# Kernel tuning notes

Measured on AMD Instinct MI355X. Metric: run time of the kernel, lower is better.

The kernel has to match this reference:

```python
import jax, jax.numpy as jnp
import numpy as np

BATCH = 2
SEQ = 2048
D_MODEL = 512
D_STATE = 16
D_CONV = 4
D_INNER = 2 * D_MODEL  # expand=2


def setup_inputs() -> dict:
    key = jax.random.key(0)
    ks = jax.random.split(key, 7)
    s = 0.02
    x = jax.random.normal(ks[0], (BATCH, SEQ, D_MODEL), jnp.float32)
    W_in = jax.random.normal(ks[1], (2 * D_INNER, D_MODEL), jnp.float32) * s
    conv_w = jax.random.normal(ks[2], (D_INNER, 1, D_CONV), jnp.float32) * s  # depthwise kernel
    conv_b = jnp.zeros((D_INNER,), jnp.float32)
    W_x = jax.random.normal(ks[3], (2 * D_STATE, D_INNER), jnp.float32) * s
    W_dt = jax.random.normal(ks[4], (D_INNER, D_INNER), jnp.float32) * s
    b_dt = jnp.zeros((D_INNER,), jnp.float32)
    # A_log init: log of [1..d_state] broadcast over d_inner rows
    A_log = jnp.log(jnp.broadcast_to(jnp.arange(1, D_STATE + 1, dtype=jnp.float32), (D_INNER, D_STATE)))
    D_param = jnp.ones((D_INNER,), jnp.float32)
    W_out = jax.random.normal(ks[5], (D_MODEL, D_INNER), jnp.float32) * s
    return dict(x=x, W_in=W_in, conv_w=conv_w, conv_b=conv_b, W_x=W_x,
                W_dt=W_dt, b_dt=b_dt, A_log=A_log, D_param=D_param, W_out=W_out)


def reference(x, W_in, conv_w, conv_b, W_x, W_dt, b_dt, A_log, D_param, W_out):
    # in_proj, split into x-branch and gate z
    xz = x @ W_in.T                             # [B, L, 2*di]
    xi, z = jnp.split(xz, 2, axis=-1)
    # depthwise causal conv1d (torch pads both sides then slices [:seq_len] == left-pad only)
    h = jnp.transpose(xi, (0, 2, 1))            # [B, di, L]
    h = jax.lax.conv_general_dilated(
        h, conv_w, window_strides=(1,), padding=[(D_CONV - 1, 0)],
        dimension_numbers=('NCH', 'OIH', 'NCH'), feature_group_count=D_INNER)
    h = h + conv_b[None, :, None]
    h = jax.nn.silu(jnp.transpose(h, (0, 2, 1)))  # [B, L, di]

    A = -jnp.exp(A_log)                         # [di, ds]
    x_dbl = h @ W_x.T                           # [B, L, 2*ds]
    _delta_unused, Bmat = jnp.split(x_dbl, 2, axis=-1)  # B (also used as C): [B, L, ds]
    delta = jax.nn.softplus(h @ W_dt.T + b_dt)  # [B, L, di] (overwrites x_proj delta, as in source)

    def step(state, inp):
        d_t, B_t, h_t = inp                     # [B,di], [B,ds], [B,di]
        dA = jnp.exp(d_t[:, :, None] * A)       # [B, di, ds]
        state = dA * state + d_t[:, :, None] * B_t[:, None, :] * h_t[:, :, None]
        y_t = jnp.einsum('bds,bs->bd', state, B_t)  # C == B
        return state, y_t

    init = jnp.zeros((x.shape[0], D_INNER, D_STATE), x.dtype)
    _, ys = jax.lax.scan(step, init,
                         (jnp.swapaxes(delta, 0, 1), jnp.swapaxes(Bmat, 0, 1), jnp.swapaxes(h, 0, 1)))
    y = jnp.swapaxes(ys, 0, 1)                  # [B, L, di]
    y = (y + D_param * h) * jax.nn.silu(z)
    return y @ W_out.T                          # [B, L, d_model]
```

## Files before the change

### kernel.cpp

```cpp
#include <hip/hip_runtime.h>
#include <cstddef>
#include <cstdint>

#define NB 2
#define L_SEQ 2048
#define DM 512
#define DS 16
#define DI 1024
#define NC 64
#define CL (L_SEQ/NC)

typedef __attribute__((ext_vector_type(4))) float f32x4;
typedef __attribute__((ext_vector_type(8))) short bf16x8;

__device__ __forceinline__ float softplus_f(float x) {
  return (x > 20.f) ? x : log1pf(expf(x));
}
__device__ __forceinline__ float silu_f(float x) {
  return x / (1.f + expf(-x));
}
__device__ __forceinline__ ushort f2bf(float f) {
  uint32_t u = __float_as_uint(f);
  return (ushort)((u + 0x7fffu + ((u >> 16) & 1u)) >> 16);
}
__device__ __forceinline__ float bf2f(ushort h) {
  return __uint_as_float(((uint32_t)h) << 16);
}

__device__ __forceinline__ void gload16(const void* g, ushort* lds_wave_base) {
  __builtin_amdgcn_global_load_lds(
      (const __attribute__((address_space(1))) void*)g,
      (__attribute__((address_space(3))) void*)lds_wave_base, 16, 0, 0);
}

template <int N>
__device__ __forceinline__ void wait_vm() {
  if constexpr (N == 0)      asm volatile("s_waitcnt vmcnt(0)" ::: "memory");
  else if constexpr (N == 3) asm volatile("s_waitcnt vmcnt(3)" ::: "memory");
  else if constexpr (N == 4) asm volatile("s_waitcnt vmcnt(4)" ::: "memory");
  else if constexpr (N == 6) asm volatile("s_waitcnt vmcnt(6)" ::: "memory");
}

__global__ __launch_bounds__(256) void split_bf16(
    const float* __restrict__ in, ushort* __restrict__ hi,
    ushort* __restrict__ lo, int n4) {
  int i = blockIdx.x * 256 + threadIdx.x;
  if (i >= n4) return;
  float4 v = ((const float4*)in)[i];
  ushort h0 = f2bf(v.x), h1 = f2bf(v.y), h2 = f2bf(v.z), h3 = f2bf(v.w);
  ((ushort4*)hi)[i] = make_ushort4(h0, h1, h2, h3);
  ((ushort4*)lo)[i] = make_ushort4(
      f2bf(v.x - bf2f(h0)), f2bf(v.y - bf2f(h1)),
      f2bf(v.z - bf2f(h2)), f2bf(v.w - bf2f(h3)));
}

template <int ACT>
__global__ __launch_bounds__(512, 4) void gemm_mfma8(
    const ushort* __restrict__ Ahi, const ushort* __restrict__ Alo, int lda,
    const ushort* __restrict__ Bhi, const ushort* __restrict__ Blo, int ldb,
    const float* __restrict__ bias, float* __restrict__ C, int ldc, int K) {
  constexpr int BM = 128, BN = 64;
  constexpr int AT = BM * 32;
  constexpr int BT = BN * 32;
  constexpr int BUF = 2 * AT + 2 * BT;
  constexpr int MR = 2, NR = 2;
  __shared__ __align__(16) ushort lds[3 * BUF];

  const int tid = threadIdx.x;
  const int lane = tid & 63;
  const int wave = tid >> 6;
  const int wr = wave >> 1;
  const int wc = wave & 1;

  const int nx = gridDim.x;
  const int nwg = nx * gridDim.y;
  int bid = blockIdx.y * nx + blockIdx.x;
  bid = (bid & 7) * (nwg >> 3) + (bid >> 3);
  const int m0 = (bid / nx) * BM;
  const int n0 = (bid % nx) * BN;

  const int ra = tid >> 2;
  const int kga = (tid & 3) ^ ((ra >> 1) & 3);
  const size_t aoff = (size_t)(m0 + ra) * lda + kga * 8;
  const int tq = tid & 255;
  const int rb = tq >> 2;
  const int kgb = (tq & 3) ^ ((rb >> 1) & 3);
  const size_t boff = (size_t)(n0 + rb) * ldb + kgb * 8;
  const ushort* Bsel = (wave < 4) ? Bhi : Blo;
  const int blds = 2 * AT + ((wave < 4) ? wave * 512 : BT + (wave - 4) * 512);

  const int fr = lane & 15, fq = lane >> 4;
  const int kswz = fq ^ ((fr >> 1) & 3);
  int aoffs[MR], boffs[NR];
#pragma unroll
  for (int m = 0; m < MR; m++) aoffs[m] = (wr * 32 + m * 16 + fr) * 32 + kswz * 8;
#pragma unroll
  for (int n = 0; n < NR; n++) boffs[n] = (wc * 32 + n * 16 + fr) * 32 + kswz * 8;

  f32x4 acc[MR][NR];
#pragma unroll
  for (int m = 0; m < MR; m++)
#pragma unroll
    for (int n = 0; n < NR; n++) acc[m][n] = (f32x4){0.f, 0.f, 0.f, 0.f};

  const int nsteps = K >> 5;

#define STAGE(base, kk)                                     \
  {                                                         \
    ushort* bp = (base);                                    \
    gload16(Ahi + aoff + (kk), bp + wave * 512);            \
    gload16(Alo + aoff + (kk), bp + AT + wave * 512);       \
    gload16(Bsel + boff + (kk), bp + blds);                 \
  }

#define COMPUTE(base)                                                          \
  {                                                                            \
    const ushort* cp = (base);                                                 \
    bf16x8 ah[MR], al[MR], bh[NR], bl[NR];                                     \
    _Pragma("unroll")                                                          \
    for (int m = 0; m < MR; m++) ah[m] = *(const bf16x8*)(cp + aoffs[m]);      \
    _Pragma("unroll")                                                          \
    for (int m = 0; m < MR; m++) al[m] = *(const bf16x8*)(cp + AT + aoffs[m]); \
    _Pragma("unroll")                                                          \
    for (int n = 0; n < NR; n++) bh[n] = *(const bf16x8*)(cp + 2 * AT + boffs[n]); \
    _Pragma("unroll")                                                          \
    for (int n = 0; n < NR; n++) bl[n] = *(const bf16x8*)(cp + 2 * AT + BT + boffs[n]); \
    _Pragma("unroll")                                                          \
    for (int m = 0; m < MR; m++)                                               \
      _Pragma("unroll")                                                        \
      for (int n = 0; n < NR; n++)                                             \
        acc[m][n] = __builtin_amdgcn_mfma_f32_16x16x32_bf16(ah[m], bh[n], acc[m][n], 0, 0, 0); \
    _Pragma("unroll")                                                          \
    for (int m = 0; m < MR; m++)                                               \
      _Pragma("unroll")                                                        \
      for (int n = 0; n < NR; n++)                                             \
        acc[m][n] = __builtin_amdgcn_mfma_f32_16x16x32_bf16(al[m], bh[n], acc[m][n], 0, 0, 0); \
    _Pragma("unroll")                                                          \
    for (int m = 0; m < MR; m++)                                               \
      _Pragma("unroll")                                                        \
      for (int n = 0; n < NR; n++)                                             \
        acc[m][n] = __builtin_amdgcn_mfma_f32_16x16x32_bf16(ah[m], bl[n], acc[m][n], 0, 0, 0); \
  }

  STAGE(lds, 0);
  STAGE(lds + BUF, 32);
  int ocur = 0, onext = BUF, ofar = 2 * BUF;
  for (int t = 0; t < nsteps; ++t) {
    if (t == nsteps - 1) wait_vm<0>(); else wait_vm<3>();
    __builtin_amdgcn_s_barrier();
    if (t + 2 < nsteps) STAGE(lds + ofar, (t + 2) << 5);
    COMPUTE(lds + ocur);
    int tmp = ocur; ocur = onext; onext = ofar; ofar = tmp;
  }
#undef STAGE
#undef COMPUTE

#pragma unroll
  for (int m = 0; m < MR; m++) {
    const int row = m0 + wr * 32 + m * 16 + fq * 4;
#pragma unroll
    for (int n = 0; n < NR; n++) {
      const int col = n0 + wc * 32 + n * 16 + fr;
      float bcol = (ACT == 1) ? bias[col] : 0.f;
#pragma unroll
      for (int j = 0; j < 4; j++) {
        float v = acc[m][n][j];
        if (ACT == 1) v = softplus_f(v + bcol);
        C[(size_t)(row + j) * ldc + col] = v;
      }
    }
  }
}

template <int BM, int BN, int ACT>
__global__ __launch_bounds__(256) void gemm_mfma4(
    const ushort* __restrict__ Ahi, const ushort* __restrict__ Alo, int lda,
    const ushort* __restrict__ Bhi, const ushort* __restrict__ Blo, int ldb,
    const float* __restrict__ bias, float* __restrict__ C, int ldc, int K) {
  constexpr int AT = BM * 32;
  constexpr int BT = BN * 32;
  constexpr int BUF = 2 * AT + 2 * BT;
  constexpr int MR = BM / 32, NR = BN / 32;
  constexpr int LPS = (BM / 64) * 2 + (BN / 64) * 2;
  __shared__ __align__(16) ushort lds[3 * BUF];

  const int tid = threadIdx.x;
  const int lane = tid & 63;
  const int wave = tid >> 6;
  const int wr = wave >> 1, wc = wave & 1;

  const int nx = gridDim.x;
  const int nwg = nx * gridDim.y;
  int bid = blockIdx.y * nx + blockIdx.x;
  bid = (bid & 7) * (nwg >> 3) + (bid >> 3);
  const int m0 = (bid / nx) * BM;
  const int n0 = (bid % nx) * BN;

  const int r0 = tid >> 2;
  const int kg = (tid & 3) ^ ((r0 >> 1) & 3);
  const size_t aoff0 = (size_t)(m0 + r0) * lda + kg * 8;
  const size_t boff0 = (size_t)(n0 + r0) * ldb + kg * 8;

  const int fr = lane & 15, fq = lane >> 4;
  const int kswz = fq ^ ((fr >> 1) & 3);
  int aoffs[MR], boffs[NR];
#pragma unroll
  for (int m = 0; m < MR; m++) aoffs[m] = (wr * (BM / 2) + m * 16 + fr) * 32 + kswz * 8;
#pragma unroll
  for (int n = 0; n < NR; n++) boffs[n] = (wc * (BN / 2) + n * 16 + fr) * 32 + kswz * 8;

  f32x4 acc[MR][NR];
#pragma unroll
  for (int m = 0; m < MR; m++)
#pragma unroll
    for (int n = 0; n < NR; n++) acc[m][n] = (f32x4){0.f, 0.f, 0.f, 0.f};

  const int nsteps = K >> 5;

#define STAGE(base, kk)                                           \
  {                                                               \
    ushort* bp = (base);                                          \
    gload16(Ahi + aoff0 + (kk), bp + wave * 512);                 \
    gload16(Alo + aoff0 + (kk), bp + AT + wave * 512);            \
    gload16(Bhi + boff0 + (kk), bp + 2 * AT + wave * 512);        \
    gload16(Blo + boff0 + (kk), bp + 2 * AT + BT + wave * 512);   \
  }

#define COMPUTE(base)                                                          \
  {                                                                            \
    const ushort* cp = (base);                                                 \
    bf16x8 ah[MR], al[MR], bh[NR], bl[NR];                                     \
    _Pragma("unroll")                                                          \
    for (int m = 0; m < MR; m++) ah[m] = *(const bf16x8*)(cp + aoffs[m]);      \
    _Pragma("unroll")                                                          \
    for (int m = 0; m < MR; m++) al[m] = *(const bf16x8*)(cp + AT + aoffs[m]); \
    _Pragma("unroll")                                                          \
    for (int n = 0; n < NR; n++) bh[n] = *(const bf16x8*)(cp + 2 * AT + boffs[n]); \
    _Pragma("unroll")                                                          \
    for (int n = 0; n < NR; n++) bl[n] = *(const bf16x8*)(cp + 2 * AT + BT + boffs[n]); \
    _Pragma("unroll")                                                          \
    for (int m = 0; m < MR; m++)                                               \
      _Pragma("unroll")                                                        \
      for (int n = 0; n < NR; n++)                                             \
        acc[m][n] = __builtin_amdgcn_mfma_f32_16x16x32_bf16(ah[m], bh[n], acc[m][n], 0, 0, 0); \
    _Pragma("unroll")                                                          \
    for (int m = 0; m < MR; m++)                                               \
      _Pragma("unroll")                                                        \
      for (int n = 0; n < NR; n++)                                             \
        acc[m][n] = __builtin_amdgcn_mfma_f32_16x16x32_bf16(al[m], bh[n], acc[m][n], 0, 0, 0); \
    _Pragma("unroll")                                                          \
    for (int m = 0; m < MR; m++)                                               \
      _Pragma("unroll")                                                        \
      for (int n = 0; n < NR; n++)                                             \
        acc[m][n] = __builtin_amdgcn_mfma_f32_16x16x32_bf16(ah[m], bl[n], acc[m][n], 0, 0, 0); \
  }

  STAGE(lds, 0);
  STAGE(lds + BUF, 32);
  int ocur = 0, onext = BUF, ofar = 2 * BUF;
  for (int t = 0; t < nsteps; ++t) {
    if (t == nsteps - 1) wait_vm<0>(); else wait_vm<LPS>();
    __builtin_amdgcn_s_barrier();
    if (t + 2 < nsteps) STAGE(lds + ofar, (t + 2) << 5);
    COMPUTE(lds + ocur);
    int tmp = ocur; ocur = onext; onext = ofar; ofar = tmp;
  }
#undef STAGE
#undef COMPUTE

#pragma unroll
  for (int m = 0; m < MR; m++) {
    const int row = m0 + wr * (BM / 2) + m * 16 + fq * 4;
#pragma unroll
    for (int n = 0; n < NR; n++) {
      const int col = n0 + wc * (BN / 2) + n * 16 + fr;
      float bcol = (ACT == 1) ? bias[col] : 0.f;
#pragma unroll
      for (int j = 0; j < 4; j++) {
        float v = acc[m][n][j];
        if (ACT == 1) v = softplus_f(v + bcol);
        C[(size_t)(row + j) * ldc + col] = v;
      }
    }
  }
}

__global__ __launch_bounds__(256) void conv_silu_kernel(
    const float* __restrict__ xz, const float* __restrict__ conv_w,
    const float* __restrict__ conv_b, float* __restrict__ h,
    ushort* __restrict__ h_hi, ushort* __restrict__ h_lo) {
  const int idx = blockIdx.x * 256 + threadIdx.x;
  const int c = idx & (DI - 1);
  const int r = idx >> 10;
  const int l = r & (L_SEQ - 1);
  const float w0 = conv_w[c * 4 + 0];
  const float w1 = conv_w[c * 4 + 1];
  const float w2 = conv_w[c * 4 + 2];
  const float w3 = conv_w[c * 4 + 3];
  const float* xp = xz + (size_t)r * (2 * DI) + c;
  float acc = conv_b[c];
  if (l >= 3) acc += xp[-3 * 2 * DI] * w0;
  if (l >= 2) acc += xp[-2 * 2 * DI] * w1;
  if (l >= 1) acc += xp[-1 * 2 * DI] * w2;
  acc += xp[0] * w3;
  const float hv = silu_f(acc);
  h[idx] = hv;
  const ushort hh = f2bf(hv);
  h_hi[idx] = hh;
  h_lo[idx] = f2bf(hv - bf2f(hh));
}

__global__ __launch_bounds__(256) void xproj_kernel(
    const float* __restrict__ h, const float* __restrict__ W_x,
    float* __restrict__ Bm) {
  const int idx = blockIdx.x * 256 + threadIdx.x;
  const int s = idx & 15;
  const int r = idx >> 4;
  const float* hp = h + (size_t)r * DI;
  const float* wp = W_x + (size_t)(DS + s) * DI;
  float acc = 0.f;
  for (int k = 0; k < DI; k += 4) {
    float4 hv = *(const float4*)(hp + k);
    float4 wv = *(const float4*)(wp + k);
    acc += hv.x * wv.x + hv.y * wv.y + hv.z * wv.z + hv.w * wv.w;
  }
  Bm[idx] = acc;
}

__global__ __launch_bounds__(256) void scan_phase1(
    const float* __restrict__ delta, const float* __restrict__ h,
    const float* __restrict__ Bm, const float* __restrict__ A_log,
    float* __restrict__ aprod, float* __restrict__ blocal) {
  __shared__ float sB[CL * DS];
  const int tid = threadIdx.x;
  const int bid = blockIdx.x;
  const int cblk = bid & 3;
  const int chunk = (bid >> 2) & (NC - 1);
  const int b = bid >> 8;
  const int c = cblk * 256 + tid;
  const size_t row0 = (size_t)b * L_SEQ + chunk * CL;
  ((float2*)sB)[tid] = ((const float2*)(Bm + row0 * DS))[tid];
  __syncthreads();

  float Acs[DS], state[DS];
#pragma unroll
  for (int s = 0; s < DS; s += 4) {
    float4 al = *(const float4*)(A_log + (size_t)c * DS + s);
    Acs[s + 0] = -__expf(al.x);
    Acs[s + 1] = -__expf(al.y);
    Acs[s + 2] = -__expf(al.z);
    Acs[s + 3] = -__expf(al.w);
    state[s + 0] = 0.f; state[s + 1] = 0.f; state[s + 2] = 0.f; state[s + 3] = 0.f;
  }
  const float* dp = delta + row0 * DI + c;
  const float* hp = h + row0 * DI + c;
  float sdt = 0.f;
  for (int t = 0; t < CL; ++t) {
    const float dt = dp[(size_t)t * DI];
    const float ht = hp[(size_t)t * DI];
    const float dth = dt * ht;
    sdt += dt;
#pragma unroll
    for (int s = 0; s < DS; ++s)
      state[s] = __expf(dt * Acs[s]) * state[s] + dth * sB[t * DS + s];
  }
  const size_t o = (((size_t)b * NC + chunk) * DI + c) * DS;
#pragma unroll
  for (int s = 0; s < DS; s += 4) {
    *(float4*)(aprod + o + s) = make_float4(
        __expf(Acs[s] * sdt), __expf(Acs[s + 1] * sdt),
        __expf(Acs[s + 2] * sdt), __expf(Acs[s + 3] * sdt));
    *(float4*)(blocal + o + s) = make_float4(state[s], state[s + 1], state[s + 2], state[s + 3]);
  }
}

__global__ __launch_bounds__(256) void scan_phase2(
    float* __restrict__ aprod, const float* __restrict__ blocal) {
  const int idx = blockIdx.x * 256 + threadIdx.x;
  const int b = idx >> 14;
  const int cs = idx & 16383;
  float st = 0.f;
  for (int ch = 0; ch < NC; ++ch) {
    const size_t o = (size_t)(b * NC + ch) * (DI * DS) + cs;
    const float a = aprod[o];
    const float bl = blocal[o];
    aprod[o] = st;
    st = a * st + bl;
  }
}

__global__ __launch_bounds__(256) void scan_phase3(
    const float* __restrict__ delta, const float* __restrict__ h,
    const float* __restrict__ Bm, const float* __restrict__ A_log,
    const float* __restrict__ sinit, float* __restrict__ xz,
    const float* __restrict__ Dp) {
  __shared__ float sB[CL * DS];
  const int tid = threadIdx.x;
  const int bid = blockIdx.x;
  const int cblk = bid & 3;
  const int chunk = (bid >> 2) & (NC - 1);
  const int b = bid >> 8;
  const int c = cblk * 256 + tid;
  const size_t row0 = (size_t)b * L_SEQ + chunk * CL;
  ((float2*)sB)[tid] = ((const float2*)(Bm + row0 * DS))[tid];
  __syncthreads();

  float Acs[DS], state[DS];
  const size_t o = (((size_t)b * NC + chunk) * DI + c) * DS;
#pragma unroll
  for (int s = 0; s < DS; s += 4) {
    float4 al = *(const float4*)(A_log + (size_t)c * DS + s);
    Acs[s + 0] = -__expf(al.x);
    Acs[s + 1] = -__expf(al.y);
    Acs[s + 2] = -__expf(al.z);
    Acs[s + 3] = -__expf(al.w);
    float4 sv = *(const float4*)(sinit + o + s);
    state[s + 0] = sv.x; state[s + 1] = sv.y; state[s + 2] = sv.z; state[s + 3] = sv.w;
  }
  const float* dp = delta + row0 * DI + c;
  const float* hp = h + row0 * DI + c;
  const float* zp = xz + row0 * (2 * DI) + DI + c;
  ushort* yrow = (ushort*)(xz + row0 * (2 * DI)) + c;
  const float Dc = Dp[c];
  for (int t = 0; t < CL; ++t) {
    const float dt = dp[(size_t)t * DI];
    const float ht = hp[(size_t)t * DI];
    const float z = zp[(size_t)t * (2 * DI)];
    const float dth = dt * ht;
    float yv = 0.f;
#pragma unroll
    for (int s = 0; s < DS; ++s) {
      const float bt = sB[t * DS + s];
      state[s] = __expf(dt * Acs[s]) * state[s] + dth * bt;
      yv += state[s] * bt;
    }
    const float g = (yv + Dc * ht) * silu_f(z);
    const ushort gh = f2bf(g);
    yrow[(size_t)t * 4096] = gh;
    yrow[(size_t)t * 4096 + 1024] = f2bf(g - bf2f(gh));
  }
}

extern "C" void kernel_launch(void* const* d_in, const int* in_sizes, int n_in,
                              void* d_out, int out_size, void* d_ws, size_t ws_size,
                              hipStream_t stream) {
  const float* x      = (const float*)d_in[0];
  const float* W_in   = (const float*)d_in[1];
  const float* conv_w = (const float*)d_in[2];
  const float* conv_b = (const float*)d_in[3];
  const float* W_x    = (const float*)d_in[4];
  const float* W_dt   = (const float*)d_in[5];
  const float* b_dt   = (const float*)d_in[6];
  const float* A_log  = (const float*)d_in[7];
  const float* D_par  = (const float*)d_in[8];
  const float* W_out  = (const float*)d_in[9];
  float* out = (float*)d_out;

  const int rows = NB * L_SEQ;

  float* xz     = (float*)d_ws;
  float* h      = xz + (size_t)(8u << 20);
  float* delta  = h + (size_t)(4u << 20);
  float* Bm     = delta + (size_t)(4u << 20);
  float* spare  = Bm + (size_t)(64u << 10);
  float* wreg   = spare + (size_t)((3u << 20) / 2);
  ushort* Wdt_hi  = (ushort*)wreg;
  ushort* Wdt_lo  = Wdt_hi + (size_t)(1u << 20);
  ushort* Wout_hi = Wdt_lo + (size_t)(1u << 20);
  ushort* Wout_lo = Wout_hi + (size_t)(512u << 10);
  float* xreg   = wreg + (size_t)((3u << 20) / 2);
  ushort* x_hi  = (ushort*)xreg;
  ushort* x_lo  = x_hi + (size_t)(2u << 20);
  ushort* Win_hi = x_lo + (size_t)(2u << 20);
  ushort* Win_lo = Win_hi + (size_t)(1u << 20);
  ushort* h_hi  = (ushort*)xreg;
  ushort* h_lo  = h_hi + (size_t)(4u << 20);
  float* aprod  = xreg;
  float* blocal = aprod + (size_t)(2u << 20);
  ushort* y_hi  = (ushort*)xz;
  ushort* y_lo  = y_hi + 1024;

  split_bf16<<<2048, 256, 0, stream>>>(x, x_hi, x_lo, rows * DM / 4);
  split_bf16<<<1024, 256, 0, stream>>>(W_in, Win_hi, Win_lo, 2 * DI * DM / 4);
  split_bf16<<<1024, 256, 0, stream>>>(W_dt, Wdt_hi, Wdt_lo, DI * DI / 4);
  split_bf16<<<512, 256, 0, stream>>>(W_out, Wout_hi, Wout_lo, DM * DI / 4);

  gemm_mfma8<0><<<dim3(32, 32), 512, 0, stream>>>(
      x_hi, x_lo, DM, Win_hi, Win_lo, DM, nullptr, xz, 2 * DI, DM);
  conv_silu_kernel<<<(rows * DI) / 256, 256, 0, stream>>>(xz, conv_w, conv_b, h, h_hi, h_lo);
  gemm_mfma8<1><<<dim3(16, 32), 512, 0, stream>>>(
      h_hi, h_lo, DI, Wdt_hi, Wdt_lo, DI, b_dt, delta, DI, DI);
  xproj_kernel<<<(rows * DS) / 256, 256, 0, stream>>>(h, W_x, Bm);
  scan_phase1<<<NB * NC * (DI / 256), 256, 0, stream>>>(delta, h, Bm, A_log, aprod, blocal);
  scan_phase2<<<(NB * DI * DS) / 256, 256, 0, stream>>>(aprod, blocal);
  scan_phase3<<<NB * NC * (DI / 256), 256, 0, stream>>>(delta, h, Bm, A_log, aprod, xz, D_par);
  gemm_mfma4<64, 64, 0><<<dim3(8, 64), 256, 0, stream>>>(
      y_hi, y_lo, 4096, Wout_hi, Wout_lo, DI, nullptr, out, DM, DI);
}
```

Before: 228.3 us.

## Fuse x_proj B-matrix into dt GEMM and switch GEMMs to double buffering

The W_x rows that produce B are appended to the split W_dt weights, and the dt GEMM grid gains one extra column tile. Its epilogue routes columns past DI into the Bm buffer, so the separate fp32 xproj kernel is removed. Both MFMA GEMM kernels also move from a 3-stage LDS pipeline with explicit vmcnt waits to a 2-stage double buffer with __syncthreads, and declare higher occupancy in launch bounds. The simpler pipeline exposes more load latency per step in exchange for lower LDS use and possibly more resident workgroups. The extra tile wastes 48 of its 64 columns and reads uninitialized weight rows whose results are discarded.

Result: faster. 208.6 us (-8.6%).

```diff
diff --git a/kernel.cpp b/kernel.cpp
--- a/kernel.cpp
+++ b/kernel.cpp
@@ -31,14 +31,6 @@
   __builtin_amdgcn_global_load_lds(
       (const __attribute__((address_space(1))) void*)g,
       (__attribute__((address_space(3))) void*)lds_wave_base, 16, 0, 0);
-}
-
-template <int N>
-__device__ __forceinline__ void wait_vm() {
-  if constexpr (N == 0)      asm volatile("s_waitcnt vmcnt(0)" ::: "memory");
-  else if constexpr (N == 3) asm volatile("s_waitcnt vmcnt(3)" ::: "memory");
-  else if constexpr (N == 4) asm volatile("s_waitcnt vmcnt(4)" ::: "memory");
-  else if constexpr (N == 6) asm volatile("s_waitcnt vmcnt(6)" ::: "memory");
 }
 
 __global__ __launch_bounds__(256) void split_bf16(
@@ -55,16 +47,17 @@
 }
 
 template <int ACT>
-__global__ __launch_bounds__(512, 4) void gemm_mfma8(
+__global__ __launch_bounds__(512, 6) void gemm_mfma8(
     const ushort* __restrict__ Ahi, const ushort* __restrict__ Alo, int lda,
     const ushort* __restrict__ Bhi, const ushort* __restrict__ Blo, int ldb,
-    const float* __restrict__ bias, float* __restrict__ C, int ldc, int K) {
+    const float* __restrict__ bias, float* __restrict__ C, int ldc,
+    float* __restrict__ Bmout, int K) {
   constexpr int BM = 128, BN = 64;
   constexpr int AT = BM * 32;
   constexpr int BT = BN * 32;
   constexpr int BUF = 2 * AT + 2 * BT;
   constexpr int MR = 2, NR = 2;
-  __shared__ __align__(16) ushort lds[3 * BUF];
+  __shared__ __align__(16) ushort lds[2 * BUF];
 
   const int tid = threadIdx.x;
   const int lane = tid & 63;
@@ -143,14 +136,11 @@
   }
 
   STAGE(lds, 0);
-  STAGE(lds + BUF, 32);
-  int ocur = 0, onext = BUF, ofar = 2 * BUF;
+  __syncthreads();
   for (int t = 0; t < nsteps; ++t) {
-    if (t == nsteps - 1) wait_vm<0>(); else wait_vm<3>();
-    __builtin_amdgcn_s_barrier();
-    if (t + 2 < nsteps) STAGE(lds + ofar, (t + 2) << 5);
-    COMPUTE(lds + ocur);
-    int tmp = ocur; ocur = onext; onext = ofar; ofar = tmp;
+    if (t + 1 < nsteps) STAGE(lds + ((t + 1) & 1) * BUF, (t + 1) << 5);
+    COMPUTE(lds + (t & 1) * BUF);
+    __syncthreads();
   }
 #undef STAGE
 #undef COMPUTE
@@ -161,28 +151,37 @@
 #pragma unroll
     for (int n = 0; n < NR; n++) {
       const int col = n0 + wc * 32 + n * 16 + fr;
-      float bcol = (ACT == 1) ? bias[col] : 0.f;
-#pragma unroll
-      for (int j = 0; j < 4; j++) {
-        float v = acc[m][n][j];
-        if (ACT == 1) v = softplus_f(v + bcol);
-        C[(size_t)(row + j) * ldc + col] = v;
+      if (ACT == 1) {
+        if (col < DI) {
+          const float bcol = bias[col];
+#pragma unroll
+          for (int j = 0; j < 4; j++)
+            C[(size_t)(row + j) * ldc + col] = softplus_f(acc[m][n][j] + bcol);
+        } else if (col < DI + DS) {
+#pragma unroll
+          for (int j = 0; j < 4; j++)
+            Bmout[(size_t)(row + j) * DS + (col - DI)] = acc[m][n][j];
+        }
+      } else {
+#pragma unroll
+        for (int j = 0; j < 4; j++)
+          C[(size_t)(row + j) * ldc + col] = acc[m][n][j];
       }
     }
   }
 }
 
-template <int BM, int BN, int ACT>
-__global__ __launch_bounds__(256) void gemm_mfma4(
+template <int ACT>
+__global__ __launch_bounds__(256, 5) void gemm_mfma4(
     const ushort* __restrict__ Ahi, const ushort* __restrict__ Alo, int lda,
     const ushort* __restrict__ Bhi, const ushort* __restrict__ Blo, int ldb,
     const float* __restrict__ bias, float* __restrict__ C, int ldc, int K) {
+  constexpr int BM = 64, BN = 64;
   constexpr int AT = BM * 32;
   constexpr int BT = BN * 32;
   constexpr int BUF = 2 * AT + 2 * BT;
-  constexpr int MR = BM / 32, NR = BN / 32;
-  constexpr int LPS = (BM / 64) * 2 + (BN / 64) * 2;
-  __shared__ __align__(16) ushort lds[3 * BUF];
+  constexpr int MR = 2, NR = 2;
+  __shared__ __align__(16) ushort lds[2 * BUF];
 
   const int tid = threadIdx.x;
   const int lane = tid & 63;
@@ -205,9 +204,9 @@
   const int kswz = fq ^ ((fr >> 1) & 3);
   int aoffs[MR], boffs[NR];
 #pragma unroll
-  for (int m = 0; m < MR; m++) aoffs[m] = (wr * (BM / 2) + m * 16 + fr) * 32 + kswz * 8;
-#pragma unroll
-  for (int n = 0; n < NR; n++) boffs[n] = (wc * (BN / 2) + n * 16 + fr) * 32 + kswz * 8;
+  for (int m = 0; m < MR; m++) aoffs[m] = (wr * 32 + m * 16 + fr) * 32 + kswz * 8;
+#pragma unroll
+  for (int n = 0; n < NR; n++) boffs[n] = (wc * 32 + n * 16 + fr) * 32 + kswz * 8;
 
   f32x4 acc[MR][NR];
 #pragma unroll
@@ -256,24 +255,21 @@
   }
 
   STAGE(lds, 0);
-  STAGE(lds + BUF, 32);
-  int ocur = 0, onext = BUF, ofar = 2 * BUF;
+  __syncthreads();
   for (int t = 0; t < nsteps; ++t) {
-    if (t == nsteps - 1) wait_vm<0>(); else wait_vm<LPS>();
-    __builtin_amdgcn_s_barrier();
-    if (t + 2 < nsteps) STAGE(lds + ofar, (t + 2) << 5);
-    COMPUTE(lds + ocur);
-    int tmp = ocur; ocur = onext; onext = ofar; ofar = tmp;
+    if (t + 1 < nsteps) STAGE(lds + ((t + 1) & 1) * BUF, (t + 1) << 5);
+    COMPUTE(lds + (t & 1) * BUF);
+    __syncthreads();
   }
 #undef STAGE
 #undef COMPUTE
 
 #pragma unroll
   for (int m = 0; m < MR; m++) {
-    const int row = m0 + wr * (BM / 2) + m * 16 + fq * 4;
+    const int row = m0 + wr * 32 + m * 16 + fq * 4;
 #pragma unroll
     for (int n = 0; n < NR; n++) {
-      const int col = n0 + wc * (BN / 2) + n * 16 + fr;
+      const int col = n0 + wc * 32 + n * 16 + fr;
       float bcol = (ACT == 1) ? bias[col] : 0.f;
 #pragma unroll
       for (int j = 0; j < 4; j++) {
@@ -310,23 +306,6 @@
   h_lo[idx] = f2bf(hv - bf2f(hh));
 }
 
-__global__ __launch_bounds__(256) void xproj_kernel(
-    const float* __restrict__ h, const float* __restrict__ W_x,
-    float* __restrict__ Bm) {
-  const int idx = blockIdx.x * 256 + threadIdx.x;
-  const int s = idx & 15;
-  const int r = idx >> 4;
-  const float* hp = h + (size_t)r * DI;
-  const float* wp = W_x + (size_t)(DS + s) * DI;
-  float acc = 0.f;
-  for (int k = 0; k < DI; k += 4) {
-    float4 hv = *(const float4*)(hp + k);
-    float4 wv = *(const float4*)(wp + k);
-    acc += hv.x * wv.x + hv.y * wv.y + hv.z * wv.z + hv.w * wv.w;
-  }
-  Bm[idx] = acc;
-}
-
 __global__ __launch_bounds__(256) void scan_phase1(
     const float* __restrict__ delta, const float* __restrict__ h,
     const float* __restrict__ Bm, const float* __restrict__ A_log,
@@ -462,13 +441,11 @@
   float* h      = xz + (size_t)(8u << 20);
   float* delta  = h + (size_t)(4u << 20);
   float* Bm     = delta + (size_t)(4u << 20);
-  float* spare  = Bm + (size_t)(64u << 10);
-  float* wreg   = spare + (size_t)((3u << 20) / 2);
-  ushort* Wdt_hi  = (ushort*)wreg;
-  ushort* Wdt_lo  = Wdt_hi + (size_t)(1u << 20);
-  ushort* Wout_hi = Wdt_lo + (size_t)(1u << 20);
+  ushort* W2hi  = (ushort*)(Bm + (size_t)(64u << 10));
+  ushort* W2lo  = W2hi + (size_t)1088 * 1024;
+  ushort* Wout_hi = W2lo + (size_t)1088 * 1024;
   ushort* Wout_lo = Wout_hi + (size_t)(512u << 10);
-  float* xreg   = wreg + (size_t)((3u << 20) / 2);
+  float* xreg   = (float*)(Wout_lo + (size_t)(512u << 10));
   ushort* x_hi  = (ushort*)xreg;
   ushort* x_lo  = x_hi + (size_t)(2u << 20);
   ushort* Win_hi = x_lo + (size_t)(2u << 20);
@@ -482,18 +459,19 @@
 
   split_bf16<<<2048, 256, 0, stream>>>(x, x_hi, x_lo, rows * DM / 4);
   split_bf16<<<1024, 256, 0, stream>>>(W_in, Win_hi, Win_lo, 2 * DI * DM / 4);
-  split_bf16<<<1024, 256, 0, stream>>>(W_dt, Wdt_hi, Wdt_lo, DI * DI / 4);
+  split_bf16<<<1024, 256, 0, stream>>>(W_dt, W2hi, W2lo, DI * DI / 4);
+  split_bf16<<<16, 256, 0, stream>>>(W_x + DS * DI,
+      W2hi + (size_t)DI * DI, W2lo + (size_t)DI * DI, DS * DI / 4);
   split_bf16<<<512, 256, 0, stream>>>(W_out, Wout_hi, Wout_lo, DM * DI / 4);
 
   gemm_mfma8<0><<<dim3(32, 32), 512, 0, stream>>>(
-      x_hi, x_lo, DM, Win_hi, Win_lo, DM, nullptr, xz, 2 * DI, DM);
+      x_hi, x_lo, DM, Win_hi, Win_lo, DM, nullptr, xz, 2 * DI, nullptr, DM);
   conv_silu_kernel<<<(rows * DI) / 256, 256, 0, stream>>>(xz, conv_w, conv_b, h, h_hi, h_lo);
-  gemm_mfma8<1><<<dim3(16, 32), 512, 0, stream>>>(
-      h_hi, h_lo, DI, Wdt_hi, Wdt_lo, DI, b_dt, delta, DI, DI);
-  xproj_kernel<<<(rows * DS) / 256, 256, 0, stream>>>(h, W_x, Bm);
+  gemm_mfma8<1><<<dim3(17, 32), 512, 0, stream>>>(
+      h_hi, h_lo, DI, W2hi, W2lo, DI, b_dt, delta, DI, Bm, DI);
   scan_phase1<<<NB * NC * (DI / 256), 256, 0, stream>>>(delta, h, Bm, A_log, aprod, blocal);
   scan_phase2<<<(NB * DI * DS) / 256, 256, 0, stream>>>(aprod, blocal);
   scan_phase3<<<NB * NC * (DI / 256), 256, 0, stream>>>(delta, h, Bm, A_log, aprod, xz, D_par);
-  gemm_mfma4<64, 64, 0><<<dim3(8, 64), 256, 0, stream>>>(
+  gemm_mfma4<0><<<dim3(8, 64), 256, 0, stream>>>(
       y_hi, y_lo, 4096, Wout_hi, Wout_lo, DI, nullptr, out, DM, DI);
 }
```
